# Performance work log

Measured on AMD Instinct MI355X. Metric: run time of the kernel, lower is better.

## Reference

```python
import jax, jax.numpy as jnp
import numpy as np

T, B, I, H, E = 32, 128, 64, 128, 4
N_TRAP = 100  # trapezoid intervals -> 101 sample points


def setup_inputs() -> dict:
    key = jax.random.key(0)
    ks = jax.random.split(key, 14)
    s_cell = 1.0 / np.sqrt(I + H)
    s_wh = 1.0 / np.sqrt((I + H) * E)

    def u(k, shape, s):
        return jax.random.uniform(k, shape, jnp.float32, -s, s)

    return {
        "x_time": jax.random.normal(ks[0], (T, B, I), jnp.float32),
        "dt_time": jax.random.uniform(ks[1], (T, B), jnp.float32, 0.01, 1.0),
        "Wh_w": u(ks[2], ((I + H) * E, H * E), s_wh),
        "Wh_b": u(ks[3], (H * E,), s_wh),
        "Wi_w": u(ks[4], (E, I + H, H), s_cell),
        "Wi_b": u(ks[5], (E, H), s_cell),
        "Wf_w": u(ks[6], (E, I + H, H), s_cell),
        "Wf_b": u(ks[7], (E, H), s_cell),
        "Wd_w": u(ks[8], (E, I + H, H), s_cell),
        "Wd_b": u(ks[9], (E, H), s_cell),
        "Wg_w": u(ks[10], (E, I + H, H), s_cell),
        "Wg_b": u(ks[11], (E, H), s_cell),
        "Wo_w": u(ks[12], (E, I + H, H), s_cell),
        "Wo_b": u(ks[13], (E, H), s_cell),
        "alpha": jnp.ones((E, H), jnp.float32) / H,
    }


def reference(x_time, dt_time, Wh_w, Wh_b, Wi_w, Wi_b, Wf_w, Wf_b,
              Wd_w, Wd_b, Wg_w, Wg_b, Wo_w, Wo_b, alpha):
    t_total, batch, in_dim = x_time.shape
    e_types, hid = alpha.shape
    ts_unit = jnp.linspace(0.0, 1.0, N_TRAP + 1, dtype=x_time.dtype)  # [101]

    def step(carry, inp):
        h, c = carry            # each [E,B,H]
        x, dt = inp             # [B,I], [B]
        # hidden_sum = Wh(cat_m([x, h_m]))
        cat = jnp.concatenate(
            [jnp.concatenate([x, h[m]], axis=-1) for m in range(e_types)], axis=-1)  # [B,(I+H)*E]
        hs = (cat @ Wh_w + Wh_b).reshape(batch, e_types, hid).transpose(1, 0, 2)     # [E,B,H]
        iv = jnp.concatenate(
            [jnp.broadcast_to(x[None], (e_types, batch, in_dim)), hs], axis=-1)       # [E,B,I+H]

        def gate(W, b):
            return jnp.einsum('ebd,edh->ebh', iv, W) + b[:, None, :]

        i_g = jax.nn.sigmoid(gate(Wi_w, Wi_b))
        f_g = jax.nn.sigmoid(gate(Wf_w, Wf_b))
        g = f_g * c + i_g * jnp.tanh(gate(Wg_w, Wg_b))   # curr_g
        delta = jnp.exp(gate(Wd_w, Wd_b))                 # curr_delta
        o = jax.nn.sigmoid(gate(Wo_w, Wo_b))              # curr_o
        diff = c - g                                      # prev_c - curr_g

        c_new = g + diff * jnp.exp(-delta * dt[None, :, None])  # c_t at dt
        h_new = o * jnp.tanh(c_new)
        lam = jnp.einsum('eh,ebh->eb', alpha, h_new)             # intensity at dt

        # trapezoidal integration of intensity over [0, dt], 100 intervals
        ts = dt[:, None] * ts_unit                                # [B,101]
        cv = g[:, :, None, :] + diff[:, :, None, :] * jnp.exp(
            -delta[:, :, None, :] * ts[None, :, :, None])         # [E,B,101,H]
        fv = jnp.einsum('eh,ebth->ebt', alpha, o[:, :, None, :] * jnp.tanh(cv))  # [E,B,101]
        integ = (dt[None, :] / N_TRAP) * (
            jnp.sum(fv, axis=-1) - 0.5 * (fv[..., 0] + fv[..., -1]))  # [E,B]

        return (h_new, c_new), (lam.T, integ.T)  # outputs [B,E]

    h0 = jnp.zeros((e_types, batch, hid), x_time.dtype)
    c0 = jnp.zeros_like(h0)
    _, (lambdas, lambda_integrals) = jax.lax.scan(step, (h0, c0), (x_time, dt_time))
    return lambdas, lambda_integrals  # each [T,B,E]
```

## Files before the change

### kernel.cpp

```cpp
#include <hip/hip_runtime.h>

#define OFF_WALL   0
#define OFF_BIAS   196608
#define OFF_WHHH   199680
#define OFF_WGH    330752
#define OFF_XG     494592
#define OFF_GST    13077504
#define OFF_HBUF   21466112
#define GST_PLANE  2097152

typedef _Float16 half2_t __attribute__((ext_vector_type(2)));

__device__ __forceinline__ float fast_sig(float x) {
    return __fdividef(1.f, 1.f + __expf(-x));
}
__device__ __forceinline__ float sig_e(float y) {
    return __builtin_amdgcn_rcpf(__expf(y) + 1.f);
}
__device__ __forceinline__ unsigned pack2h(float a, float b) {
    _Float16 ha = (_Float16)a, hb = (_Float16)b;
    unsigned short ua = __builtin_bit_cast(unsigned short, ha);
    unsigned short ub = __builtin_bit_cast(unsigned short, hb);
    return ((unsigned)ub << 16) | ua;
}
__device__ __forceinline__ float dot2(unsigned w, unsigned h, float acc) {
    return __builtin_amdgcn_fdot2(__builtin_bit_cast(half2_t, w),
                                  __builtin_bit_cast(half2_t, h), acc, false);
}

__global__ __launch_bounds__(256) void k0_pack(
    const float* __restrict__ Wh_w, const float* __restrict__ Wh_b,
    const float* __restrict__ Wi_w, const float* __restrict__ Wi_b,
    const float* __restrict__ Wf_w, const float* __restrict__ Wf_b,
    const float* __restrict__ Wd_w, const float* __restrict__ Wd_b,
    const float* __restrict__ Wg_w, const float* __restrict__ Wg_b,
    const float* __restrict__ Wo_w, const float* __restrict__ Wo_b,
    float* __restrict__ ws)
{
    const float* gw[5] = {Wi_w, Wf_w, Wd_w, Wg_w, Wo_w};
    const float* gb[5] = {Wi_b, Wf_b, Wd_b, Wg_b, Wo_b};
    int idx = blockIdx.x * 256 + threadIdx.x;
    if (idx < 196608) {
        int r = idx / 3072, col = idx - r * 3072;
        float v;
        if (col < 512) {
            v = Wh_w[r * 512 + col] + Wh_w[(192 + r) * 512 + col]
              + Wh_w[(384 + r) * 512 + col] + Wh_w[(576 + r) * 512 + col];
        } else {
            int q = col - 512;
            int e = q / 640;
            int rem = q - e * 640;
            int g = rem >> 7, h = rem & 127;
            v = gw[g][(e * 192 + r) * 128 + h];
        }
        ws[OFF_WALL + idx] = v;
    } else if (idx < 327680) {
        int i = idx - 196608;
        int q    = i & 3;
        int lane = (i >> 2) & 127;
        int i4   = (i >> 9) & 15;
        int kq   = (i >> 13) & 3;
        int e    = i >> 15;
        int kp = i4 * 4 + q;
        int k0 = kq * 128 + 2 * kp;
        int r0 = (k0 >> 7) * 192 + 64 + (k0 & 127);
        float w0 = Wh_w[r0 * 512 + e * 128 + lane];
        float w1 = Wh_w[(r0 + 1) * 512 + e * 128 + lane];
        reinterpret_cast<unsigned*>(ws + OFF_WHHH)[i] = pack2h(w0, w1);
    } else if (idx < 491520) {
        int i = idx - 327680;
        int lane = i & 127;
        int gg = (i >> 7) % 5;
        int rest = (i >> 7) / 5;
        int ii = rest & 15;
        int kq = (rest >> 4) & 3;
        int e  = rest >> 6;
        int k0 = kq * 32 + 2 * ii, k1 = k0 + 1;
        float w0 = gw[gg][(e * 192 + 64 + k0) * 128 + lane];
        float w1 = gw[gg][(e * 192 + 64 + k1) * 128 + lane];
        reinterpret_cast<unsigned*>(ws + OFF_WGH)[i] = pack2h(w0, w1);
    }
    if (idx < 3072) {
        float v;
        if (idx < 512) v = Wh_b[idx];
        else {
            int q = idx - 512;
            int e = q / 640;
            int rem = q - e * 640;
            int g = rem >> 7, h = rem & 127;
            v = gb[g][e * 128 + h];
        }
        ws[OFF_BIAS + idx] = v;
    }
    if (idx < 262144) {
        reinterpret_cast<unsigned*>(ws + OFF_HBUF)[idx] = 0xFFFFFFFFu;
    }
}

__global__ __launch_bounds__(256) void k1_xproj(
    const float* __restrict__ x, const float* wsr, float* XG)
{
    __shared__ __align__(16) float XT[64 * 68];
    const float* W_all = wsr + OFF_WALL;
    const float* bias  = wsr + OFF_BIAS;
    int bid = blockIdx.x;
    int ct = bid % 48, rt = bid / 48;
    int r0 = rt * 64, c0 = ct * 64;
    for (int p = threadIdx.x; p < 4096; p += 256) {
        int i = p >> 6, k = p & 63;
        XT[k * 68 + i] = x[(r0 + i) * 64 + k];
    }
    __syncthreads();
    int col = c0 + (threadIdx.x & 63);
    int iq = threadIdx.x >> 6;
    float acc[16];
    #pragma unroll
    for (int r = 0; r < 16; r++) acc[r] = 0.f;
    const float* wp = W_all + col;
    #pragma unroll 4
    for (int k = 0; k < 64; k++) {
        float w = wp[k * 3072];
        const float4* xt4 = reinterpret_cast<const float4*>(&XT[k * 68 + iq * 16]);
        #pragma unroll
        for (int r4 = 0; r4 < 4; r4++) {
            float4 xv = xt4[r4];
            acc[r4 * 4 + 0] = fmaf(xv.x, w, acc[r4 * 4 + 0]);
            acc[r4 * 4 + 1] = fmaf(xv.y, w, acc[r4 * 4 + 1]);
            acc[r4 * 4 + 2] = fmaf(xv.z, w, acc[r4 * 4 + 2]);
            acc[r4 * 4 + 3] = fmaf(xv.w, w, acc[r4 * 4 + 3]);
        }
    }
    float bv = bias[col];
    #pragma unroll
    for (int r = 0; r < 16; r++) {
        int row = r0 + iq * 16 + r;
        XG[row * 3072 + col] = acc[r] + bv;
    }
}

__global__ __launch_bounds__(512, 1) void k2_recur(
    const uint4* __restrict__ WhhH4,
    const unsigned* __restrict__ WgH,
    const float* __restrict__ XG,
    const float* __restrict__ dt_time,
    const float* __restrict__ alpha,
    float* __restrict__ Gst,
    unsigned* __restrict__ hbuf,
    float* __restrict__ lam_out)
{
    __shared__ __align__(16) uint4 waL[8192];
    __shared__ __align__(16) unsigned hsP[2][64];
    __shared__ __align__(16) unsigned hOut[128];
    __shared__ float pA[4][2][128];
    __shared__ float pB[4][2][5][128];
    __shared__ float red[4];
    const int tid = threadIdx.x;
    const int bid = blockIdx.x;
    const int e   = (bid >> 3) & 3;
    const int grp = (bid & 7) | ((bid >> 5) << 3);
    const int b0  = grp * 2;
    const int kq  = tid >> 7;
    const int lane = tid & 127;
    const int l64 = tid & 63;
    const int s = (tid >> 7) & 1, l = lane;

    {
        const uint4* src = WhhH4 + (size_t)e * 8192;
        #pragma unroll
        for (int n = 0; n < 16; ++n) waL[tid + 512 * n] = src[tid + 512 * n];
    }
    unsigned wg[5][16];
    #pragma unroll
    for (int i = 0; i < 16; i++) {
        #pragma unroll
        for (int g = 0; g < 5; g++)
            wg[g][i] = WgH[(((e * 4 + kq) * 16 + i) * 5 + g) * 128 + lane];
    }
    const float av = alpha[e * 128 + lane];
    float cst = 0.f;
    __syncthreads();

    for (int t = 0; t < 32; ++t) {
        const int row0 = t * 128 + b0;
        float xg0 = 0.f, xgg0 = 0.f, xgg1 = 0.f, xgg2 = 0.f, xgg3 = 0.f, xgg4 = 0.f;
        if (tid < 256) {
            const float* base = XG + (size_t)(row0 + s) * 3072;
            xg0 = base[e * 128 + l];
            const float* gp = base + 512 + e * 640 + l;
            xgg0 = gp[0]; xgg1 = gp[128]; xgg2 = gp[256]; xgg3 = gp[384]; xgg4 = gp[512];
        }
        if (t > 0) {
            uint2 hu;
            if (kq == e) {
                hu.x = hOut[l64];
                hu.y = hOut[64 + l64];
            } else {
                const unsigned long long* ap =
                    reinterpret_cast<const unsigned long long*>(
                        hbuf + ((size_t)((t & 1) * 64 + grp) * 4 + e) * 512)
                    + (kq * 64 + l64);
                unsigned long long v = __hip_atomic_load(ap, __ATOMIC_RELAXED,
                                                         __HIP_MEMORY_SCOPE_AGENT);
                while (v == ~0ull) {
                    __builtin_amdgcn_s_sleep(1);
                    v = __hip_atomic_load(ap, __ATOMIC_RELAXED,
                                          __HIP_MEMORY_SCOPE_AGENT);
                }
                hu.x = (unsigned)v;
                hu.y = (unsigned)(v >> 32);
            }
            float a0 = 0.f, a1 = 0.f;
            #pragma unroll
            for (int i4 = 0; i4 < 16; ++i4) {
                uint4 w = waL[(kq * 16 + i4) * 128 + lane];
                unsigned h0, h1;
                h0 = __builtin_amdgcn_readlane(hu.x, i4 * 4 + 0);
                h1 = __builtin_amdgcn_readlane(hu.y, i4 * 4 + 0);
                a0 = dot2(w.x, h0, a0); a1 = dot2(w.x, h1, a1);
                h0 = __builtin_amdgcn_readlane(hu.x, i4 * 4 + 1);
                h1 = __builtin_amdgcn_readlane(hu.y, i4 * 4 + 1);
                a0 = dot2(w.y, h0, a0); a1 = dot2(w.y, h1, a1);
                h0 = __builtin_amdgcn_readlane(hu.x, i4 * 4 + 2);
                h1 = __builtin_amdgcn_readlane(hu.y, i4 * 4 + 2);
                a0 = dot2(w.z, h0, a0); a1 = dot2(w.z, h1, a1);
                h0 = __builtin_amdgcn_readlane(hu.x, i4 * 4 + 3);
                h1 = __builtin_amdgcn_readlane(hu.y, i4 * 4 + 3);
                a0 = dot2(w.w, h0, a0); a1 = dot2(w.w, h1, a1);
            }
            pA[kq][0][lane] = a0;
            pA[kq][1][lane] = a1;
        }
        __syncthreads();
        if (t > 0 && kq != e && lane < 64) {
            unsigned long long* ap =
                reinterpret_cast<unsigned long long*>(
                    hbuf + ((size_t)((t & 1) * 64 + grp) * 4 + e) * 512)
                + (kq * 64 + l64);
            __hip_atomic_store(ap, ~0ull, __ATOMIC_RELAXED, __HIP_MEMORY_SCOPE_AGENT);
        }
        if (tid < 256) {
            float hs = xg0;
            if (t > 0) hs += pA[0][s][l] + pA[1][s][l] + pA[2][s][l] + pA[3][s][l];
            float hi = __shfl_down(hs, 1, 64);
            if ((l & 1) == 0) hsP[s][l >> 1] = pack2h(hs, hi);
        }
        __syncthreads();
        float b0a = 0.f, b1a = 0.f, b2a = 0.f, b3a = 0.f, b4a = 0.f;
        float b0b = 0.f, b1b = 0.f, b2b = 0.f, b3b = 0.f, b4b = 0.f;
        {
            unsigned hv = hsP[(l64 >> 4) & 1][kq * 16 + (l64 & 15)];
            #pragma unroll
            for (int i = 0; i < 16; ++i) {
                unsigned h0 = __builtin_amdgcn_readlane(hv, i);
                unsigned h1 = __builtin_amdgcn_readlane(hv, 16 + i);
                b0a = dot2(wg[0][i], h0, b0a); b0b = dot2(wg[0][i], h1, b0b);
                b1a = dot2(wg[1][i], h0, b1a); b1b = dot2(wg[1][i], h1, b1b);
                b2a = dot2(wg[2][i], h0, b2a); b2b = dot2(wg[2][i], h1, b2b);
                b3a = dot2(wg[3][i], h0, b3a); b3b = dot2(wg[3][i], h1, b3b);
                b4a = dot2(wg[4][i], h0, b4a); b4b = dot2(wg[4][i], h1, b4b);
            }
        }
        pB[kq][0][0][lane] = b0a; pB[kq][0][1][lane] = b1a; pB[kq][0][2][lane] = b2a;
        pB[kq][0][3][lane] = b3a; pB[kq][0][4][lane] = b4a;
        pB[kq][1][0][lane] = b0b; pB[kq][1][1][lane] = b1b; pB[kq][1][2][lane] = b2b;
        pB[kq][1][3][lane] = b3b; pB[kq][1][4][lane] = b4b;
        __syncthreads();
        if (tid < 256) {
            float ai = pB[0][s][0][l] + pB[1][s][0][l] + pB[2][s][0][l] + pB[3][s][0][l] + xgg0;
            float af = pB[0][s][1][l] + pB[1][s][1][l] + pB[2][s][1][l] + pB[3][s][1][l] + xgg1;
            float ad = pB[0][s][2][l] + pB[1][s][2][l] + pB[2][s][2][l] + pB[3][s][2][l] + xgg2;
            float ag = pB[0][s][3][l] + pB[1][s][3][l] + pB[2][s][3][l] + pB[3][s][3][l] + xgg3;
            float ao = pB[0][s][4][l] + pB[1][s][4][l] + pB[2][s][4][l] + pB[3][s][4][l] + xgg4;
            float ig = fast_sig(ai);
            float fg = fast_sig(af);
            float dl = __expf(ad);
            float gt = tanhf(ag);
            float og = fast_sig(ao);
            float gc = fmaf(fg, cst, ig * gt);
            float df = cst - gc;
            float dtv = dt_time[row0 + s];
            cst = fmaf(df, __expf(-dl * dtv), gc);
            float hn = og * tanhf(cst);
            size_t go = (size_t)(row0 + s) * 512 + e * 128 + l;
            Gst[0 * GST_PLANE + go] = gc;
            Gst[1 * GST_PLANE + go] = df;
            Gst[2 * GST_PLANE + go] = dl;
            Gst[3 * GST_PLANE + go] = og;
            float hi = __shfl_down(hn, 1, 64);
            if ((l & 1) == 0) hOut[s * 64 + (l >> 1)] = pack2h(hn, hi);
            float lm = av * hn;
            #pragma unroll
            for (int off = 32; off > 0; off >>= 1) lm += __shfl_down(lm, off, 64);
            if ((tid & 63) == 0) red[tid >> 6] = lm;
        }
        __syncthreads();
        if (tid == 0) {
            lam_out[(row0 + 0) * 4 + e] = red[0] + red[1];
            lam_out[(row0 + 1) * 4 + e] = red[2] + red[3];
        }
        if (tid < 192) {
            int cpy = tid >> 6;
            cpy += (cpy >= e) ? 1 : 0;
            int qp = tid & 63;
            unsigned long long v =
                ((unsigned long long)hOut[64 + qp] << 32) | (unsigned long long)hOut[qp];
            unsigned long long* dst =
                reinterpret_cast<unsigned long long*>(
                    hbuf + ((size_t)(((t + 1) & 1) * 64 + grp) * 4 + cpy) * 512)
                + (e * 64 + qp);
            __hip_atomic_store(dst, v, __ATOMIC_RELAXED, __HIP_MEMORY_SCOPE_AGENT);
        }
    }
}

__global__ __launch_bounds__(256) void k3_trap(
    const float* __restrict__ Gst, const float* __restrict__ dt_time,
    const float* __restrict__ alpha, float* __restrict__ integ_out)
{
    __shared__ float red[4][2];
    const int row = blockIdx.x;
    const int tid = threadIdx.x;
    const float dtv = dt_time[row];
    const int base = row * 512;
    const int iA = tid, iB = tid + 256;
    float gcA = Gst[0 * GST_PLANE + base + iA];
    float gcB = Gst[0 * GST_PLANE + base + iB];
    float dfA = Gst[1 * GST_PLANE + base + iA];
    float dfB = Gst[1 * GST_PLANE + base + iB];
    float dlA = Gst[2 * GST_PLANE + base + iA];
    float dlB = Gst[2 * GST_PLANE + base + iB];
    float oA  = Gst[3 * GST_PLANE + base + iA];
    float oB  = Gst[3 * GST_PLANE + base + iB];
    float aoA = alpha[iA] * oA;
    float aoB = alpha[iB] * oB;
    float gA = 2.f * gcA, dA = 2.f * dfA;
    float gB = 2.f * gcB, dB = 2.f * dfB;
    float qA = dlA * dtv, qB = dlB * dtv;
    float r1A = __expf(-qA * 0.01f), r1B = __expf(-qB * 0.01f);
    float r2A = r1A * r1A, r2B = r1B * r1B;
    float r4A = r2A * r2A, r4B = r2B * r2B;
    float e100A = __expf(-qA), e100B = __expf(-qB);
    float sA = 0.5f * sig_e(gA + dA) - 0.5f * sig_e(fmaf(dA, e100A, gA));
    float sB = 0.5f * sig_e(gB + dB) - 0.5f * sig_e(fmaf(dB, e100B, gB));
    float E1A = r1A, E2A = r2A, E3A = r2A * r1A, E4A = r4A;
    float E1B = r1B, E2B = r2B, E3B = r2B * r1B, E4B = r4B;
    float s1A = 0.f, s2A = 0.f, s3A = 0.f, s4A = 0.f;
    float s1B = 0.f, s2B = 0.f, s3B = 0.f, s4B = 0.f;
    #pragma unroll
    for (int k = 0; k < 25; ++k) {
        s1A += sig_e(fmaf(dA, E1A, gA)); E1A *= r4A;
        s1B += sig_e(fmaf(dB, E1B, gB)); E1B *= r4B;
        s2A += sig_e(fmaf(dA, E2A, gA)); E2A *= r4A;
        s2B += sig_e(fmaf(dB, E2B, gB)); E2B *= r4B;
        s3A += sig_e(fmaf(dA, E3A, gA)); E3A *= r4A;
        s3B += sig_e(fmaf(dB, E3B, gB)); E3B *= r4B;
        s4A += sig_e(fmaf(dA, E4A, gA)); E4A *= r4A;
        s4B += sig_e(fmaf(dB, E4B, gB)); E4B *= r4B;
    }
    sA += (s1A + s2A) + (s3A + s4A);
    sB += (s1B + s2B) + (s3B + s4B);
    float vA = aoA * (100.f - 2.f * sA);
    float vB = aoB * (100.f - 2.f * sB);
    #pragma unroll
    for (int off = 32; off > 0; off >>= 1) {
        vA += __shfl_down(vA, off, 64);
        vB += __shfl_down(vB, off, 64);
    }
    const int wv = tid >> 6;
    if ((tid & 63) == 0) { red[wv][0] = vA; red[wv][1] = vB; }
    __syncthreads();
    if (tid < 4) {
        float v = (tid < 2) ? (red[2 * tid][0] + red[2 * tid + 1][0])
                            : (red[2 * (tid - 2)][1] + red[2 * (tid - 2) + 1][1]);
        integ_out[row * 4 + tid] = v * (dtv * 0.01f);
    }
}

extern "C" void kernel_launch(void* const* d_in, const int* in_sizes, int n_in,
                              void* d_out, int out_size, void* d_ws, size_t ws_size,
                              hipStream_t stream)
{
    const float* x_time  = (const float*)d_in[0];
    const float* dt_time = (const float*)d_in[1];
    const float* Wh_w = (const float*)d_in[2];
    const float* Wh_b = (const float*)d_in[3];
    const float* Wi_w = (const float*)d_in[4];
    const float* Wi_b = (const float*)d_in[5];
    const float* Wf_w = (const float*)d_in[6];
    const float* Wf_b = (const float*)d_in[7];
    const float* Wd_w = (const float*)d_in[8];
    const float* Wd_b = (const float*)d_in[9];
    const float* Wg_w = (const float*)d_in[10];
    const float* Wg_b = (const float*)d_in[11];
    const float* Wo_w = (const float*)d_in[12];
    const float* Wo_b = (const float*)d_in[13];
    const float* alpha = (const float*)d_in[14];

    float* ws = (float*)d_ws;
    float* XG   = ws + OFF_XG;
    float* Gst  = ws + OFF_GST;
    unsigned* hbuf = (unsigned*)(ws + OFF_HBUF);
    float* lam_out   = (float*)d_out;
    float* integ_out = lam_out + 32 * 128 * 4;

    k0_pack<<<3072, 256, 0, stream>>>(Wh_w, Wh_b, Wi_w, Wi_b, Wf_w, Wf_b,
                                      Wd_w, Wd_b, Wg_w, Wg_b, Wo_w, Wo_b, ws);
    k1_xproj<<<3072, 256, 0, stream>>>(x_time, ws, XG);
    k2_recur<<<256, 512, 0, stream>>>(
        (const uint4*)(ws + OFF_WHHH), (const unsigned*)(ws + OFF_WGH),
        XG, dt_time, alpha, Gst, hbuf, lam_out);
    k3_trap<<<4096, 256, 0, stream>>>(Gst, dt_time, alpha, integ_out);
}
```

Before: 212.6 us.

## Fuse trapezoid integration into recurrent kernel, dropping the gate-state buffer

Removes the separate trapezoid kernel and the global gate-state buffer. Each recurrence step now keeps the cell state in shared memory, and all 512 threads compute the sigmoid sum, splitting the 101 sample points into two halves so idle threads take part. This avoids global writes and reads of four planes and one kernel launch. The cost is extra serial work on the recurrence critical path every time step, which runs on only 256 blocks instead of the highly parallel 4096-block launch.

```diff
diff --git a/kernel.cpp b/kernel.cpp
--- a/kernel.cpp
+++ b/kernel.cpp
@@ -5,9 +5,7 @@
 #define OFF_WHHH   199680
 #define OFF_WGH    330752
 #define OFF_XG     494592
-#define OFF_GST    13077504
 #define OFF_HBUF   21466112
-#define GST_PLANE  2097152
 
 typedef _Float16 half2_t __attribute__((ext_vector_type(2)));
 
@@ -144,16 +142,18 @@
     const float* __restrict__ XG,
     const float* __restrict__ dt_time,
     const float* __restrict__ alpha,
-    float* __restrict__ Gst,
     unsigned* __restrict__ hbuf,
-    float* __restrict__ lam_out)
+    float* __restrict__ lam_out,
+    float* __restrict__ integ_out)
 {
     __shared__ __align__(16) uint4 waL[8192];
     __shared__ __align__(16) unsigned hsP[2][64];
     __shared__ __align__(16) unsigned hOut[128];
     __shared__ float pA[4][2][128];
     __shared__ float pB[4][2][5][128];
+    __shared__ __align__(16) float4 cellSt[256];
     __shared__ float red[4];
+    __shared__ float red2[8];
     const int tid = threadIdx.x;
     const int bid = blockIdx.x;
     const int e   = (bid >> 3) & 3;
@@ -281,11 +281,9 @@
             float dtv = dt_time[row0 + s];
             cst = fmaf(df, __expf(-dl * dtv), gc);
             float hn = og * tanhf(cst);
-            size_t go = (size_t)(row0 + s) * 512 + e * 128 + l;
-            Gst[0 * GST_PLANE + go] = gc;
-            Gst[1 * GST_PLANE + go] = df;
-            Gst[2 * GST_PLANE + go] = dl;
-            Gst[3 * GST_PLANE + go] = og;
+            float4 stv;
+            stv.x = 2.f * gc; stv.y = 2.f * df; stv.z = dl * dtv; stv.w = av * og;
+            cellSt[tid] = stv;
             float hi = __shfl_down(hn, 1, 64);
             if ((l & 1) == 0) hOut[s * 64 + (l >> 1)] = pack2h(hn, hi);
             float lm = av * hn;
@@ -310,69 +308,52 @@
                 + (e * 64 + qp);
             __hip_atomic_store(dst, v, __ATOMIC_RELAXED, __HIP_MEMORY_SCOPE_AGENT);
         }
-    }
-}
-
-__global__ __launch_bounds__(256) void k3_trap(
-    const float* __restrict__ Gst, const float* __restrict__ dt_time,
-    const float* __restrict__ alpha, float* __restrict__ integ_out)
-{
-    __shared__ float red[4][2];
-    const int row = blockIdx.x;
-    const int tid = threadIdx.x;
-    const float dtv = dt_time[row];
-    const int base = row * 512;
-    const int iA = tid, iB = tid + 256;
-    float gcA = Gst[0 * GST_PLANE + base + iA];
-    float gcB = Gst[0 * GST_PLANE + base + iB];
-    float dfA = Gst[1 * GST_PLANE + base + iA];
-    float dfB = Gst[1 * GST_PLANE + base + iB];
-    float dlA = Gst[2 * GST_PLANE + base + iA];
-    float dlB = Gst[2 * GST_PLANE + base + iB];
-    float oA  = Gst[3 * GST_PLANE + base + iA];
-    float oB  = Gst[3 * GST_PLANE + base + iB];
-    float aoA = alpha[iA] * oA;
-    float aoB = alpha[iB] * oB;
-    float gA = 2.f * gcA, dA = 2.f * dfA;
-    float gB = 2.f * gcB, dB = 2.f * dfB;
-    float qA = dlA * dtv, qB = dlB * dtv;
-    float r1A = __expf(-qA * 0.01f), r1B = __expf(-qB * 0.01f);
-    float r2A = r1A * r1A, r2B = r1B * r1B;
-    float r4A = r2A * r2A, r4B = r2B * r2B;
-    float e100A = __expf(-qA), e100B = __expf(-qB);
-    float sA = 0.5f * sig_e(gA + dA) - 0.5f * sig_e(fmaf(dA, e100A, gA));
-    float sB = 0.5f * sig_e(gB + dB) - 0.5f * sig_e(fmaf(dB, e100B, gB));
-    float E1A = r1A, E2A = r2A, E3A = r2A * r1A, E4A = r4A;
-    float E1B = r1B, E2B = r2B, E3B = r2B * r1B, E4B = r4B;
-    float s1A = 0.f, s2A = 0.f, s3A = 0.f, s4A = 0.f;
-    float s1B = 0.f, s2B = 0.f, s3B = 0.f, s4B = 0.f;
-    #pragma unroll
-    for (int k = 0; k < 25; ++k) {
-        s1A += sig_e(fmaf(dA, E1A, gA)); E1A *= r4A;
-        s1B += sig_e(fmaf(dB, E1B, gB)); E1B *= r4B;
-        s2A += sig_e(fmaf(dA, E2A, gA)); E2A *= r4A;
-        s2B += sig_e(fmaf(dB, E2B, gB)); E2B *= r4B;
-        s3A += sig_e(fmaf(dA, E3A, gA)); E3A *= r4A;
-        s3B += sig_e(fmaf(dB, E3B, gB)); E3B *= r4B;
-        s4A += sig_e(fmaf(dA, E4A, gA)); E4A *= r4A;
-        s4B += sig_e(fmaf(dB, E4B, gB)); E4B *= r4B;
-    }
-    sA += (s1A + s2A) + (s3A + s4A);
-    sB += (s1B + s2B) + (s3B + s4B);
-    float vA = aoA * (100.f - 2.f * sA);
-    float vB = aoB * (100.f - 2.f * sB);
-    #pragma unroll
-    for (int off = 32; off > 0; off >>= 1) {
-        vA += __shfl_down(vA, off, 64);
-        vB += __shfl_down(vB, off, 64);
-    }
-    const int wv = tid >> 6;
-    if ((tid & 63) == 0) { red[wv][0] = vA; red[wv][1] = vB; }
-    __syncthreads();
-    if (tid < 4) {
-        float v = (tid < 2) ? (red[2 * tid][0] + red[2 * tid + 1][0])
-                            : (red[2 * (tid - 2)][1] + red[2 * (tid - 2) + 1][1]);
-        integ_out[row * 4 + tid] = v * (dtv * 0.01f);
+        {
+            const int x = tid & 255;
+            float4 stv = cellSt[x];
+            float g2 = stv.x, d2 = stv.y, q = stv.z, ao = stv.w;
+            float r  = __expf(-0.01f * q);
+            float r2 = r * r, r4 = r2 * r2;
+            float T;
+            if (tid < 256) {
+                float E1 = r, E2 = r2, E3 = r2 * r, E4 = r4;
+                float s1 = 0.f, s2 = 0.f, s3 = 0.f, s4 = 0.f;
+                #pragma unroll
+                for (int k = 0; k < 12; ++k) {
+                    s1 += sig_e(fmaf(d2, E1, g2)); E1 *= r4;
+                    s2 += sig_e(fmaf(d2, E2, g2)); E2 *= r4;
+                    s3 += sig_e(fmaf(d2, E3, g2)); E3 *= r4;
+                    s4 += sig_e(fmaf(d2, E4, g2)); E4 *= r4;
+                }
+                float sg0 = sig_e(g2 + d2);
+                T = 48.5f - 2.f * ((s1 + s2) + (s3 + s4)) - sg0;
+            } else {
+                float E49 = __expf(-0.49f * q);
+                float E1 = E49, E2 = E49 * r, E3 = E49 * r2, E4 = E49 * r2 * r;
+                float s1 = 0.f, s2 = 0.f, s3 = 0.f, s4 = 0.f;
+                #pragma unroll
+                for (int k = 0; k < 13; ++k) {
+                    s1 += sig_e(fmaf(d2, E1, g2)); E1 *= r4;
+                    s2 += sig_e(fmaf(d2, E2, g2)); E2 *= r4;
+                    s3 += sig_e(fmaf(d2, E3, g2)); E3 *= r4;
+                    s4 += sig_e(fmaf(d2, E4, g2)); E4 *= r4;
+                }
+                float e100 = __expf(-q);
+                float sg100 = sig_e(fmaf(d2, e100, g2));
+                T = 51.5f - 2.f * ((s1 + s2) + (s3 + s4)) + sg100;
+            }
+            float v = ao * T;
+            #pragma unroll
+            for (int off = 32; off > 0; off >>= 1) v += __shfl_down(v, off, 64);
+            if ((tid & 63) == 0) red2[tid >> 6] = v;
+        }
+        __syncthreads();
+        if (tid < 2) {
+            float dtv = dt_time[row0 + tid];
+            float v = (tid == 0) ? (red2[0] + red2[1] + red2[4] + red2[5])
+                                 : (red2[2] + red2[3] + red2[6] + red2[7]);
+            integ_out[(row0 + tid) * 4 + e] = v * (dtv * 0.01f);
+        }
     }
 }
 
@@ -398,7 +379,6 @@
 
     float* ws = (float*)d_ws;
     float* XG   = ws + OFF_XG;
-    float* Gst  = ws + OFF_GST;
     unsigned* hbuf = (unsigned*)(ws + OFF_HBUF);
     float* lam_out   = (float*)d_out;
     float* integ_out = lam_out + 32 * 128 * 4;
@@ -408,6 +388,5 @@
     k1_xproj<<<3072, 256, 0, stream>>>(x_time, ws, XG);
     k2_recur<<<256, 512, 0, stream>>>(
         (const uint4*)(ws + OFF_WHHH), (const unsigned*)(ws + OFF_WGH),
-        XG, dt_time, alpha, Gst, hbuf, lam_out);
-    k3_trap<<<4096, 256, 0, stream>>>(Gst, dt_time, alpha, integ_out);
-}
+        XG, dt_time, alpha, hbuf, lam_out, integ_out);
+}
```

Measured after the change: 212.3 us. Within noise of the previous version (-0.2%).
